# Kernel optimization log

Measured on AMD Instinct MI355X. Metric: run time of the kernel, lower is better.

Reference implementation:

```python
import jax, jax.numpy as jnp
import numpy as np

D_MODEL = 2048
N_HEAD = 16
D_HEAD = D_MODEL // N_HEAD


def setup_inputs() -> dict:
    key = jax.random.key(0)
    k_x, k_qkv, k_proj = jax.random.split(key, 3)
    x = jax.random.normal(k_x, (2, 2048, D_MODEL), dtype=jnp.float32)
    # nn.Linear weights: out = x @ W.T ; store as [out, in] like torch
    scale = 1.0 / np.sqrt(D_MODEL)
    W_qkv = jax.random.uniform(k_qkv, (3 * D_MODEL, D_MODEL), jnp.float32, -scale, scale)
    W_proj = jax.random.uniform(k_proj, (D_MODEL, D_MODEL), jnp.float32, -scale, scale)
    return {"x": x, "W_qkv": W_qkv, "W_proj": W_proj}


def reference(x, W_qkv, W_proj):
    B, T, C = x.shape
    qkv = jnp.einsum('btc,oc->bto', x, W_qkv)  # [B,T,3C]
    q, k, v = jnp.split(qkv, 3, axis=-1)
    def heads(t):
        return t.reshape(B, T, N_HEAD, D_HEAD).transpose(0, 2, 1, 3)  # [B,H,T,Dh]
    q, k, v = heads(q), heads(k), heads(v)
    att = jnp.einsum('bhqd,bhkd->bhqk', q, k) / jnp.sqrt(jnp.float32(D_HEAD))
    causal = jnp.tril(jnp.ones((T, T), dtype=bool))  # True = keep
    att = jnp.where(causal, att, -jnp.inf)
    att = jax.nn.softmax(att, axis=-1)
    y = jnp.einsum('bhqk,bhkd->bhqd', att, v)
    y = y.transpose(0, 2, 1, 3).reshape(B, T, C)
    return jnp.einsum('btc,oc->bto', y, W_proj)
```

## Files before the change

kernel.cpp:

```cpp
#include <hip/hip_runtime.h>
#include <hip/hip_bf16.h>
#include <stdint.h>


typedef __bf16 bf16x8 __attribute__((ext_vector_type(8)));
typedef float f32x4 __attribute__((ext_vector_type(4)));
typedef unsigned short u16x8 __attribute__((ext_vector_type(8)));
typedef unsigned short u16x4 __attribute__((ext_vector_type(4)));

__device__ __forceinline__ unsigned short f2bf(float f) {
  unsigned int u = __builtin_bit_cast(unsigned int, f);
  u += 0x7fff + ((u >> 16) & 1);
  return (unsigned short)(u >> 16);
}
__device__ __forceinline__ float bf2f(unsigned short u) {
  return __builtin_bit_cast(float, (unsigned int)u << 16);
}

__device__ __forceinline__ u16x8 cvt8(const float* p) {
  f32x4 lo = *(const f32x4*)p;
  f32x4 hi = *(const f32x4*)(p + 4);
  u16x8 r;
#pragma unroll
  for (int j = 0; j < 4; j++) { r[j] = f2bf(lo[j]); r[4 + j] = f2bf(hi[j]); }
  return r;
}

__device__ __forceinline__ void gload16(const void* g, void* l) {
  __builtin_amdgcn_global_load_lds(
      (const __attribute__((address_space(1))) void*)g,
      (__attribute__((address_space(3))) void*)l, 16, 0, 0);
}

__global__ __launch_bounds__(256) void f32_to_bf16(
    const float* __restrict__ src, unsigned short* __restrict__ dst, int n8) {
  int i = blockIdx.x * 256 + threadIdx.x;
  const int stride = gridDim.x * 256;
  for (; i < n8; i += stride) {
    u16x8 v = cvt8(src + (size_t)i * 8);
    *(u16x8*)&dst[(size_t)i * 8] = v;
  }
}

template <bool COF32>
__global__ __launch_bounds__(256) void gemm_bf(
    const unsigned short* __restrict__ A, const unsigned short* __restrict__ B,
    void* __restrict__ Cv, int M, int N, int K) {
  __shared__ __align__(16) unsigned short Alds[128 * 32];
  __shared__ __align__(16) unsigned short Blds[128 * 32];

  const int tid  = threadIdx.x;
  const int lane = tid & 63;
  const int w    = tid >> 6;
  const int ln   = lane & 15;
  const int kq   = lane >> 4;
  const int m0 = blockIdx.y * 128;
  const int n0 = blockIdx.x * 128;
  const int m_base = (w >> 1) * 64;
  const int n_base = (w & 1) * 64;

  f32x4 acc[4][4];
#pragma unroll
  for (int i = 0; i < 4; i++)
#pragma unroll
    for (int j = 0; j < 4; j++) acc[i][j] = {0.f, 0.f, 0.f, 0.f};

  const int c0 = tid;
  const int c1 = tid + 256;
  const unsigned short* Ag0 = A + (size_t)(m0 + (c0 >> 2)) * K + (c0 & 3) * 8;
  const unsigned short* Ag1 = A + (size_t)(m0 + (c1 >> 2)) * K + (c1 & 3) * 8;
  const unsigned short* Bg0 = B + (size_t)(n0 + (c0 >> 2)) * K + (c0 & 3) * 8;
  const unsigned short* Bg1 = B + (size_t)(n0 + (c1 >> 2)) * K + (c1 & 3) * 8;
  unsigned short* lA0 = &Alds[(size_t)w * 512];
  unsigned short* lA1 = &Alds[2048 + (size_t)w * 512];
  unsigned short* lB0 = &Blds[(size_t)w * 512];
  unsigned short* lB1 = &Blds[2048 + (size_t)w * 512];

  const int nk = K >> 5;
  for (int kt = 0; kt < nk; kt++) {
    const int ko = kt * 32;
    gload16(Ag0 + ko, lA0);
    gload16(Ag1 + ko, lA1);
    gload16(Bg0 + ko, lB0);
    gload16(Bg1 + ko, lB1);
    __syncthreads();

    bf16x8 af[4], bfr[4];
#pragma unroll
    for (int i = 0; i < 4; i++)
      af[i] = *(const bf16x8*)&Alds[(m_base + i * 16 + ln) * 32 + kq * 8];
#pragma unroll
    for (int j = 0; j < 4; j++)
      bfr[j] = *(const bf16x8*)&Blds[(n_base + j * 16 + ln) * 32 + kq * 8];
#pragma unroll
    for (int i = 0; i < 4; i++)
#pragma unroll
      for (int j = 0; j < 4; j++)
        acc[i][j] = __builtin_amdgcn_mfma_f32_16x16x32_bf16(af[i], bfr[j], acc[i][j], 0, 0, 0);
    __syncthreads();
  }

#pragma unroll
  for (int i = 0; i < 4; i++) {
    const int row_base = m0 + m_base + i * 16 + kq * 4;
#pragma unroll
    for (int j = 0; j < 4; j++) {
      const int col = n0 + n_base + j * 16 + ln;
#pragma unroll
      for (int r = 0; r < 4; r++) {
        const size_t idx = (size_t)(row_base + r) * N + col;
        if (COF32) ((float*)Cv)[idx] = acc[i][j][r];
        else       ((unsigned short*)Cv)[idx] = f2bf(acc[i][j][r]);
      }
    }
  }
}

template <bool COF32>
__global__ __launch_bounds__(512, 2) void gemm8(
    const unsigned short* __restrict__ A, const unsigned short* __restrict__ B,
    void* __restrict__ Cv, int M, int N, int K) {
  __shared__ __align__(1024) unsigned short As[2][16384];
  __shared__ __align__(1024) unsigned short Bs[2][16384];

  const int tid  = threadIdx.x;
  const int lane = tid & 63;
  const int w    = tid >> 6;
  const int ln   = lane & 15;
  const int kq   = lane >> 4;
  const int wm   = w >> 2;
  const int wn   = w & 3;
  const int m0 = blockIdx.y * 256;
  const int n0 = blockIdx.x * 256;

  const int kswz = (kq * 8) ^ ((ln & 8) << 1);

  const int lx = lane ^ (((lane >> 5) & 1) << 1);
  const int srow = w * 16 + (lx >> 2);
  const int scol = (lx & 3) * 8;
  const unsigned short* Asrc = A + (size_t)(m0 + srow) * K + scol;
  const unsigned short* Bsrc = B + (size_t)(n0 + srow) * K + scol;

  f32x4 acc[8][4];
#pragma unroll
  for (int i = 0; i < 8; i++)
#pragma unroll
    for (int j = 0; j < 4; j++) acc[i][j] = {0.f, 0.f, 0.f, 0.f};

  auto stgA = [&](int buf, int t, int h) {
    const size_t off = (size_t)t * 64 + (size_t)(h * 128) * K;
    gload16(Asrc + off,      &As[buf][h * 4096 + w * 512]);
    gload16(Asrc + off + 32, &As[buf][8192 + h * 4096 + w * 512]);
  };
  auto stgB = [&](int buf, int t, int h) {
    const size_t off = (size_t)t * 64 + (size_t)(h * 128) * K;
    gload16(Bsrc + off,      &Bs[buf][h * 4096 + w * 512]);
    gload16(Bsrc + off + 32, &Bs[buf][8192 + h * 4096 + w * 512]);
  };
  auto rdA = [&](int buf, int mi, int ks) -> bf16x8 {
    return *(const bf16x8*)&As[buf][ks * 8192 + (wm * 128 + mi * 16 + ln) * 32 + kswz];
  };
  auto rdB = [&](int buf, int nj, int ks) -> bf16x8 {
    return *(const bf16x8*)&Bs[buf][ks * 8192 + (wn * 64 + nj * 16 + ln) * 32 + kswz];
  };

  const int NT = K >> 6;

  stgA(0, 0, 0); stgA(0, 0, 1); stgB(0, 0, 0); stgB(0, 0, 1);
  stgA(1, 1, 0); stgA(1, 1, 1);
  asm volatile("s_waitcnt vmcnt(4)" ::: "memory");
  __builtin_amdgcn_s_barrier();

  bf16x8 a0[4][2], a1[4][2], b01[2][2], b23[2][2];

#pragma unroll 2
  for (int t = 0; t < NT; t++) {
    const int cur = t & 1, nxt = cur ^ 1;

#pragma unroll
    for (int i = 0; i < 4; i++) { a0[i][0] = rdA(cur, i, 0); a0[i][1] = rdA(cur, i, 1); }
#pragma unroll
    for (int j = 0; j < 2; j++) { b01[j][0] = rdB(cur, j, 0); b01[j][1] = rdB(cur, j, 1); }
    if (t + 1 < NT) stgB(nxt, t + 1, 0);
    asm volatile("s_waitcnt lgkmcnt(8)" ::: "memory");
    __builtin_amdgcn_s_barrier();
    asm volatile("s_waitcnt lgkmcnt(0)" ::: "memory");
    __builtin_amdgcn_sched_barrier(0);
    __builtin_amdgcn_s_setprio(1);
#pragma unroll
    for (int i = 0; i < 4; i++)
#pragma unroll
      for (int j = 0; j < 2; j++) {
        acc[i][j] = __builtin_amdgcn_mfma_f32_16x16x32_bf16(a0[i][0], b01[j][0], acc[i][j], 0, 0, 0);
        acc[i][j] = __builtin_amdgcn_mfma_f32_16x16x32_bf16(a0[i][1], b01[j][1], acc[i][j], 0, 0, 0);
      }
    __builtin_amdgcn_s_setprio(0);
    __builtin_amdgcn_s_barrier();

#pragma unroll
    for (int j = 0; j < 2; j++) { b23[j][0] = rdB(cur, 2 + j, 0); b23[j][1] = rdB(cur, 2 + j, 1); }
    if (t + 1 < NT) stgB(nxt, t + 1, 1);
    __builtin_amdgcn_s_barrier();
    asm volatile("s_waitcnt lgkmcnt(0)" ::: "memory");
    __builtin_amdgcn_sched_barrier(0);
    __builtin_amdgcn_s_setprio(1);
#pragma unroll
    for (int i = 0; i < 4; i++)
#pragma unroll
      for (int j = 0; j < 2; j++) {
        acc[i][2 + j] = __builtin_amdgcn_mfma_f32_16x16x32_bf16(a0[i][0], b23[j][0], acc[i][2 + j], 0, 0, 0);
        acc[i][2 + j] = __builtin_amdgcn_mfma_f32_16x16x32_bf16(a0[i][1], b23[j][1], acc[i][2 + j], 0, 0, 0);
      }
    __builtin_amdgcn_s_setprio(0);
    __builtin_amdgcn_s_barrier();

#pragma unroll
    for (int i = 0; i < 4; i++) { a1[i][0] = rdA(cur, 4 + i, 0); a1[i][1] = rdA(cur, 4 + i, 1); }
    asm volatile("s_waitcnt lgkmcnt(4)" ::: "memory");
    __builtin_amdgcn_s_barrier();
    asm volatile("s_waitcnt lgkmcnt(0)" ::: "memory");
    __builtin_amdgcn_sched_barrier(0);
    __builtin_amdgcn_s_setprio(1);
#pragma unroll
    for (int i = 0; i < 4; i++)
#pragma unroll
      for (int j = 0; j < 2; j++) {
        acc[4 + i][2 + j] = __builtin_amdgcn_mfma_f32_16x16x32_bf16(a1[i][0], b23[j][0], acc[4 + i][2 + j], 0, 0, 0);
        acc[4 + i][2 + j] = __builtin_amdgcn_mfma_f32_16x16x32_bf16(a1[i][1], b23[j][1], acc[4 + i][2 + j], 0, 0, 0);
      }
    __builtin_amdgcn_s_setprio(0);
    __builtin_amdgcn_s_barrier();

    if (t + 2 < NT) { stgA(cur, t + 2, 0); stgA(cur, t + 2, 1); }
    __builtin_amdgcn_s_barrier();
    __builtin_amdgcn_sched_barrier(0);
    __builtin_amdgcn_s_setprio(1);
#pragma unroll
    for (int i = 0; i < 4; i++)
#pragma unroll
      for (int j = 0; j < 2; j++) {
        acc[4 + i][j] = __builtin_amdgcn_mfma_f32_16x16x32_bf16(a1[i][0], b01[j][0], acc[4 + i][j], 0, 0, 0);
        acc[4 + i][j] = __builtin_amdgcn_mfma_f32_16x16x32_bf16(a1[i][1], b01[j][1], acc[4 + i][j], 0, 0, 0);
      }
    __builtin_amdgcn_s_setprio(0);
    if (t + 2 < NT) asm volatile("s_waitcnt vmcnt(4)" ::: "memory");
    else            asm volatile("s_waitcnt vmcnt(0)" ::: "memory");
    __builtin_amdgcn_s_barrier();
  }

#pragma unroll
  for (int mi = 0; mi < 8; mi++) {
    const int row_base = m0 + wm * 128 + mi * 16 + kq * 4;
#pragma unroll
    for (int nj = 0; nj < 4; nj++) {
      const int col = n0 + wn * 64 + nj * 16 + ln;
#pragma unroll
      for (int r = 0; r < 4; r++) {
        const size_t idx = (size_t)(row_base + r) * N + col;
        if (COF32) ((float*)Cv)[idx] = acc[mi][nj][r];
        else       ((unsigned short*)Cv)[idx] = f2bf(acc[mi][nj][r]);
      }
    }
  }
}

#define TSEQ 2048
#define CDIM 2048
#define QKVLD 6144
#define DH 128
#define NEG_BIG (-1.0e30f)
#define K_LD 136
#define VT_LD 76
#define P_LD 72

__global__ __launch_bounds__(512, 4) void attn(
    const unsigned short* __restrict__ qkv,
    unsigned short* __restrict__ y) {
  __shared__ __align__(16) unsigned short Klds[64 * K_LD];
  __shared__ __align__(16) unsigned short Vt[DH * VT_LD];
  __shared__ __align__(16) unsigned short Plds[8 * 16 * P_LD];

  const int tid  = threadIdx.x;
  const int lane = tid & 63;
  const int w    = tid >> 6;
  const int ln   = lane & 15;
  const int kq   = lane >> 4;

  const int idx  = blockIdx.x;
  const int half = idx >> 8;
  const int qbi  = idx & 15;
  const int qb   = half ? qbi : 15 - qbi;
  const int h    = (idx >> 4) & 15;
  const int b    = half;
  const int q0   = qb * 128;
  const int qrow = q0 + w * 16 + ln;

  const size_t baseQ = (size_t)b * TSEQ * QKVLD + (size_t)h * DH;
  const size_t baseK = baseQ + CDIM;
  const size_t baseV = baseQ + 2 * CDIM;

  bf16x8 qf[4];
  {
    const float scale = 0.08838834764831845f;
    const unsigned short* qp = qkv + baseQ + (size_t)qrow * QKVLD + kq * 8;
#pragma unroll
    for (int kc = 0; kc < 4; kc++) {
      u16x8 raw = *(const u16x8*)(qp + kc * 32);
      u16x8 t;
#pragma unroll
      for (int j = 0; j < 8; j++) t[j] = f2bf(bf2f(raw[j]) * scale);
      qf[kc] = __builtin_bit_cast(bf16x8, t);
    }
  }

  const int kRow = tid >> 4;
  const int kCol = (tid & 15) * 8;
  const int vK4  = (tid & 15) * 4;
  const int vD0  = (tid >> 4) * 4;
  const unsigned short* Kg = qkv + baseK + (size_t)kRow * QKVLD + kCol;
  const unsigned short* Vg = qkv + baseV + (size_t)vK4 * QKVLD + vD0;

  u16x8 kreg[2];
  u16x4 vreg[4];
#pragma unroll
  for (int it = 0; it < 2; it++)
    kreg[it] = *(const u16x8*)(Kg + (size_t)(it * 32) * QKVLD);
#pragma unroll
  for (int r = 0; r < 4; r++)
    vreg[r] = *(const u16x4*)(Vg + (size_t)r * QKVLD);

  f32x4 o[8];
#pragma unroll
  for (int i = 0; i < 8; i++) o[i] = {0.f, 0.f, 0.f, 0.f};
  float m = NEG_BIG, l = 0.f;
  unsigned short* pw = &Plds[w * 16 * P_LD];

  const int ktEnd   = 2 * qb + 2;
  const int myKtMax = (q0 + w * 16) >> 6;

  for (int kt = 0; kt < ktEnd; kt++) {
    __syncthreads();

#pragma unroll
    for (int it = 0; it < 2; it++)
      *(u16x8*)&Klds[(kRow + it * 32) * K_LD + kCol] = kreg[it];
#pragma unroll
    for (int j = 0; j < 4; j++) {
      u16x4 t = {vreg[0][j], vreg[1][j], vreg[2][j], vreg[3][j]};
      *(u16x4*)&Vt[(vD0 + j) * VT_LD + vK4] = t;
    }
    __syncthreads();

    if (kt + 1 < ktEnd) {
      const size_t off = (size_t)(kt + 1) * 64 * QKVLD;
#pragma unroll
      for (int it = 0; it < 2; it++)
        kreg[it] = *(const u16x8*)(Kg + off + (size_t)(it * 32) * QKVLD);
#pragma unroll
      for (int r = 0; r < 4; r++)
        vreg[r] = *(const u16x4*)(Vg + off + (size_t)r * QKVLD);
    }

    if (kt > myKtMax) continue;

    f32x4 s[4];
#pragma unroll
    for (int nt = 0; nt < 4; nt++) {
      s[nt] = {0.f, 0.f, 0.f, 0.f};
#pragma unroll
      for (int kc = 0; kc < 4; kc++) {
        bf16x8 kb = *(const bf16x8*)&Klds[(nt * 16 + ln) * K_LD + kc * 32 + kq * 8];
        s[nt] = __builtin_amdgcn_mfma_f32_16x16x32_bf16(kb, qf[kc], s[nt], 0, 0, 0);
      }
    }

    if (kt == myKtMax) {
      const int kbase = kt * 64 + kq * 4;
#pragma unroll
      for (int nt = 0; nt < 4; nt++)
#pragma unroll
        for (int r = 0; r < 4; r++)
          if (kbase + nt * 16 + r > qrow) s[nt][r] = NEG_BIG;
    }

    float mt;
    {
      f32x4 t01 = {fmaxf(s[0][0], s[0][1]), fmaxf(s[0][2], s[0][3]),
                   fmaxf(s[1][0], s[1][1]), fmaxf(s[1][2], s[1][3])};
      f32x4 t23 = {fmaxf(s[2][0], s[2][1]), fmaxf(s[2][2], s[2][3]),
                   fmaxf(s[3][0], s[3][1]), fmaxf(s[3][2], s[3][3])};
      f32x4 t = {fmaxf(t01[0], t01[1]), fmaxf(t01[2], t01[3]),
                 fmaxf(t23[0], t23[1]), fmaxf(t23[2], t23[3])};
      mt = fmaxf(fmaxf(t[0], t[1]), fmaxf(t[2], t[3]));
    }
    mt = fmaxf(mt, __shfl_xor(mt, 16, 64));
    mt = fmaxf(mt, __shfl_xor(mt, 32, 64));

    const bool defer = __all(mt - m <= 8.0f);
    const float mn = defer ? m : fmaxf(m, mt);
    const float alpha = defer ? 1.0f : __expf(m - mn);
    m = mn;

    float ps = 0.f;
#pragma unroll
    for (int nt = 0; nt < 4; nt++) {
      u16x4 pbits;
#pragma unroll
      for (int r = 0; r < 4; r++) {
        const float p = __expf(s[nt][r] - mn);
        ps += p;
        pbits[r] = f2bf(p);
      }
      *(u16x4*)&pw[ln * P_LD + nt * 16 + kq * 4] = pbits;
    }
    ps += __shfl_xor(ps, 16, 64);
    ps += __shfl_xor(ps, 32, 64);
    l = l * alpha + ps;

    if (!defer) {
#pragma unroll
      for (int i = 0; i < 8; i++)
#pragma unroll
        for (int r = 0; r < 4; r++) o[i][r] *= alpha;
    }

    bf16x8 pa[2];
#pragma unroll
    for (int kc = 0; kc < 2; kc++)
      pa[kc] = *(const bf16x8*)&pw[ln * P_LD + kc * 32 + kq * 8];
#pragma unroll
    for (int nt = 0; nt < 8; nt++)
#pragma unroll
      for (int kc = 0; kc < 2; kc++) {
        bf16x8 vb = *(const bf16x8*)&Vt[(nt * 16 + ln) * VT_LD + kc * 32 + kq * 8];
        o[nt] = __builtin_amdgcn_mfma_f32_16x16x32_bf16(vb, pa[kc], o[nt], 0, 0, 0);
      }
  }

  const float inv = 1.f / l;
  unsigned short* yp = y + (size_t)(b * TSEQ + qrow) * CDIM + (size_t)h * DH + kq * 4;
#pragma unroll
  for (int nt = 0; nt < 8; nt++) {
    u16x4 ov;
#pragma unroll
    for (int r = 0; r < 4; r++) ov[r] = f2bf(o[nt][r] * inv);
    *(u16x4*)(yp + nt * 16) = ov;
  }
}

extern "C" void kernel_launch(void* const* d_in, const int* in_sizes, int n_in,
                              void* d_out, int out_size, void* d_ws, size_t ws_size,
                              hipStream_t stream) {
  const float* x     = (const float*)d_in[0];
  const float* Wqkv  = (const float*)d_in[1];
  const float* Wproj = (const float*)d_in[2];
  void* out = d_out;

  unsigned short* qkv = (unsigned short*)d_ws;
  unsigned short* y   = qkv + (size_t)4096 * 6144;
  unsigned short* xbf = y;
  unsigned short* wbf = y + (size_t)4096 * 2048;

  f32_to_bf16<<<dim3(2048), 256, 0, stream>>>(x, xbf, (4096 * 2048) / 8);
  f32_to_bf16<<<dim3(2048), 256, 0, stream>>>(Wqkv, wbf, (6144 * 2048) / 8);
  gemm8<false><<<dim3(24, 16), 512, 0, stream>>>(xbf, wbf, qkv, 4096, 6144, 2048);
  f32_to_bf16<<<dim3(2048), 256, 0, stream>>>(Wproj, wbf, (2048 * 2048) / 8);
  attn<<<dim3(512), 512, 0, stream>>>(qkv, y);
  gemm_bf<true><<<dim3(16, 32), 256, 0, stream>>>(y, wbf, out, 4096, 2048, 2048);
}
```

Measured before the change: 385.1 us.

## Rewrite attention with 32x32 MFMA, register P, swizzled double-buffered LDS

```diff
diff --git a/kernel.cpp b/kernel.cpp
--- a/kernel.cpp
+++ b/kernel.cpp
@@ -5,8 +5,10 @@
 
 typedef __bf16 bf16x8 __attribute__((ext_vector_type(8)));
 typedef float f32x4 __attribute__((ext_vector_type(4)));
+typedef float f32x16 __attribute__((ext_vector_type(16)));
 typedef unsigned short u16x8 __attribute__((ext_vector_type(8)));
 typedef unsigned short u16x4 __attribute__((ext_vector_type(4)));
+typedef unsigned int u32x4v __attribute__((ext_vector_type(4)));
 
 __device__ __forceinline__ unsigned short f2bf(float f) {
   unsigned int u = __builtin_bit_cast(unsigned int, f);
@@ -269,22 +271,18 @@
 #define QKVLD 6144
 #define DH 128
 #define NEG_BIG (-1.0e30f)
-#define K_LD 136
-#define VT_LD 76
-#define P_LD 72
-
-__global__ __launch_bounds__(512, 4) void attn(
+
+__global__ __launch_bounds__(256, 2) void attn(
     const unsigned short* __restrict__ qkv,
     unsigned short* __restrict__ y) {
-  __shared__ __align__(16) unsigned short Klds[64 * K_LD];
-  __shared__ __align__(16) unsigned short Vt[DH * VT_LD];
-  __shared__ __align__(16) unsigned short Plds[8 * 16 * P_LD];
+  __shared__ __align__(1024) unsigned short Klds[2][8192];
+  __shared__ __align__(1024) unsigned short Vt[2][8192];
 
   const int tid  = threadIdx.x;
   const int lane = tid & 63;
   const int w    = tid >> 6;
-  const int ln   = lane & 15;
-  const int kq   = lane >> 4;
+  const int l5   = lane & 31;
+  const int hi   = lane >> 5;
 
   const int idx  = blockIdx.x;
   const int half = idx >> 8;
@@ -293,159 +291,199 @@
   const int h    = (idx >> 4) & 15;
   const int b    = half;
   const int q0   = qb * 128;
-  const int qrow = q0 + w * 16 + ln;
+  const int qcol = q0 + w * 32 + l5;
 
   const size_t baseQ = (size_t)b * TSEQ * QKVLD + (size_t)h * DH;
   const size_t baseK = baseQ + CDIM;
   const size_t baseV = baseQ + 2 * CDIM;
 
-  bf16x8 qf[4];
+  bf16x8 qf[8];
   {
     const float scale = 0.08838834764831845f;
-    const unsigned short* qp = qkv + baseQ + (size_t)qrow * QKVLD + kq * 8;
-#pragma unroll
-    for (int kc = 0; kc < 4; kc++) {
-      u16x8 raw = *(const u16x8*)(qp + kc * 32);
+    const unsigned short* qp = qkv + baseQ + (size_t)qcol * QKVLD + hi * 8;
+#pragma unroll
+    for (int c = 0; c < 8; c++) {
+      u16x8 raw = *(const u16x8*)(qp + c * 16);
       u16x8 t;
 #pragma unroll
       for (int j = 0; j < 8; j++) t[j] = f2bf(bf2f(raw[j]) * scale);
-      qf[kc] = __builtin_bit_cast(bf16x8, t);
-    }
-  }
-
-  const int kRow = tid >> 4;
-  const int kCol = (tid & 15) * 8;
-  const int vK4  = (tid & 15) * 4;
-  const int vD0  = (tid >> 4) * 4;
-  const unsigned short* Kg = qkv + baseK + (size_t)kRow * QKVLD + kCol;
-  const unsigned short* Vg = qkv + baseV + (size_t)vK4 * QKVLD + vD0;
-
-  u16x8 kreg[2];
-  u16x4 vreg[4];
-#pragma unroll
-  for (int it = 0; it < 2; it++)
-    kreg[it] = *(const u16x8*)(Kg + (size_t)(it * 32) * QKVLD);
-#pragma unroll
-  for (int r = 0; r < 4; r++)
-    vreg[r] = *(const u16x4*)(Vg + (size_t)r * QKVLD);
-
-  f32x4 o[8];
-#pragma unroll
-  for (int i = 0; i < 8; i++) o[i] = {0.f, 0.f, 0.f, 0.f};
+      qf[c] = __builtin_bit_cast(bf16x8, t);
+    }
+  }
+
+  const int kkeyb = tid >> 4;
+  const int kslot = tid & 15;
+  const int vk4 = (tid & 15) * 4;
+  const int vd8 = (tid >> 4) * 8;
+  const unsigned short* Vgb = qkv + baseV + (size_t)vk4 * QKVLD + vd8;
+
+  u16x8 vreg[4];
+
+  auto stageK = [&](int buf, int kt) {
+#pragma unroll
+    for (int it = 0; it < 4; it++) {
+      const int key = it * 16 + kkeyb;
+      const unsigned short* src = qkv + baseK + (size_t)(kt * 64 + key) * QKVLD
+                                + (size_t)((kslot ^ (key & 7)) * 8);
+      gload16(src, (char*)&Klds[buf][0] + it * 4096 + w * 1024);
+    }
+  };
+  auto loadV = [&](int kt) {
+    const size_t off = (size_t)kt * 64 * QKVLD;
+#pragma unroll
+    for (int r = 0; r < 4; r++)
+      vreg[r] = *(const u16x8*)(Vgb + off + (size_t)r * QKVLD);
+  };
+  auto writeV = [&](int buf) {
+#pragma unroll
+    for (int j = 0; j < 8; j++) {
+      const int d = vd8 + j;
+      u16x4 t4 = {vreg[0][j], vreg[1][j], vreg[2][j], vreg[3][j]};
+      *(u16x4*)((char*)&Vt[buf][0] + d * 128 + ((vk4 * 2) ^ ((d & 7) << 4))) = t4;
+    }
+  };
+  auto rdK = [&](int buf, int ks, int c) -> bf16x8 {
+    const int key = ks * 32 + l5;
+    return *(const bf16x8*)((const char*)&Klds[buf][0] + key * 256 +
+                            ((c * 32 + hi * 16) ^ ((key & 7) << 4)));
+  };
+  auto rdV = [&](int buf, int ds, int kc) -> bf16x8 {
+    const int d = ds * 32 + l5;
+    return *(const bf16x8*)((const char*)&Vt[buf][0] + d * 128 +
+                            ((kc * 32 + hi * 16) ^ ((d & 7) << 4)));
+  };
+
+  f32x16 o[4];
+#pragma unroll
+  for (int ds = 0; ds < 4; ds++)
+#pragma unroll
+    for (int r = 0; r < 16; r++) o[ds][r] = 0.f;
   float m = NEG_BIG, l = 0.f;
-  unsigned short* pw = &Plds[w * 16 * P_LD];
 
   const int ktEnd   = 2 * qb + 2;
-  const int myKtMax = (q0 + w * 16) >> 6;
+  const int myKtMax = (q0 + w * 32) >> 6;
+
+  stageK(0, 0);
+  loadV(0);
+  writeV(0);
+  __syncthreads();
 
   for (int kt = 0; kt < ktEnd; kt++) {
+    const int buf = kt & 1;
+    const bool pre = (kt + 1 < ktEnd);
+    if (pre) { stageK(buf ^ 1, kt + 1); loadV(kt + 1); }
+
+    if (kt <= myKtMax) {
+      f32x16 s0, s1;
+#pragma unroll
+      for (int r = 0; r < 16; r++) { s0[r] = 0.f; s1[r] = 0.f; }
+      __builtin_amdgcn_s_setprio(1);
+#pragma unroll
+      for (int c = 0; c < 8; c++) {
+        bf16x8 k0 = rdK(buf, 0, c);
+        bf16x8 k1 = rdK(buf, 1, c);
+        s0 = __builtin_amdgcn_mfma_f32_32x32x16_bf16(k0, qf[c], s0, 0, 0, 0);
+        s1 = __builtin_amdgcn_mfma_f32_32x32x16_bf16(k1, qf[c], s1, 0, 0, 0);
+      }
+      __builtin_amdgcn_s_setprio(0);
+
+      if (kt == myKtMax) {
+        const int kb0 = kt * 64 + 4 * hi;
+#pragma unroll
+        for (int r = 0; r < 16; r++) {
+          const int row = (r & 3) + 8 * (r >> 2) + kb0;
+          if (row > qcol)      s0[r] = NEG_BIG;
+          if (row + 32 > qcol) s1[r] = NEG_BIG;
+        }
+      }
+
+      float mt = s0[0];
+#pragma unroll
+      for (int r = 1; r < 16; r++) mt = fmaxf(mt, s0[r]);
+#pragma unroll
+      for (int r = 0; r < 16; r++) mt = fmaxf(mt, s1[r]);
+      mt = fmaxf(mt, __shfl_xor(mt, 32, 64));
+
+      const bool defer = __all(mt - m <= 8.0f);
+      const float mn = defer ? m : fmaxf(m, mt);
+      const float alpha = defer ? 1.0f : __expf(m - mn);
+      m = mn;
+
+      float ps = 0.f;
+      unsigned int w0[2][4], w1[2][4];
+#pragma unroll
+      for (int g = 0; g < 4; g++) {
+        float p0 = __expf(s0[4 * g + 0] - mn), p1 = __expf(s0[4 * g + 1] - mn);
+        float p2 = __expf(s0[4 * g + 2] - mn), p3 = __expf(s0[4 * g + 3] - mn);
+        ps += (p0 + p1) + (p2 + p3);
+        w0[0][g] = (unsigned)f2bf(p0) | ((unsigned)f2bf(p1) << 16);
+        w1[0][g] = (unsigned)f2bf(p2) | ((unsigned)f2bf(p3) << 16);
+      }
+#pragma unroll
+      for (int g = 0; g < 4; g++) {
+        float p0 = __expf(s1[4 * g + 0] - mn), p1 = __expf(s1[4 * g + 1] - mn);
+        float p2 = __expf(s1[4 * g + 2] - mn), p3 = __expf(s1[4 * g + 3] - mn);
+        ps += (p0 + p1) + (p2 + p3);
+        w0[1][g] = (unsigned)f2bf(p0) | ((unsigned)f2bf(p1) << 16);
+        w1[1][g] = (unsigned)f2bf(p2) | ((unsigned)f2bf(p3) << 16);
+      }
+      ps += __shfl_xor(ps, 32, 64);
+      l = l * alpha + ps;
+
+      if (!defer) {
+#pragma unroll
+        for (int ds = 0; ds < 4; ds++)
+#pragma unroll
+          for (int r = 0; r < 16; r++) o[ds][r] *= alpha;
+      }
+
+      unsigned int pw0[2][4], pw1[2][4];
+#pragma unroll
+      for (int ks = 0; ks < 2; ks++)
+#pragma unroll
+        for (int g = 0; g < 4; g++) {
+          pw0[ks][g] = (unsigned)__shfl_xor((int)w0[ks][g], 32, 64);
+          pw1[ks][g] = (unsigned)__shfl_xor((int)w1[ks][g], 32, 64);
+        }
+      bf16x8 pf[4];
+#pragma unroll
+      for (int kc = 0; kc < 4; kc++) {
+        const int ks = kc >> 1;
+        const int g = ((kc & 1) << 1) | hi;
+        u32x4v fw;
+        fw[0] = hi ? pw0[ks][g] : w0[ks][g];
+        fw[1] = hi ? pw1[ks][g] : w1[ks][g];
+        fw[2] = hi ? w0[ks][g] : pw0[ks][g];
+        fw[3] = hi ? w1[ks][g] : pw1[ks][g];
+        pf[kc] = __builtin_bit_cast(bf16x8, fw);
+      }
+
+      __builtin_amdgcn_s_setprio(1);
+#pragma unroll
+      for (int ds = 0; ds < 4; ds++)
+#pragma unroll
+        for (int kc = 0; kc < 4; kc++) {
+          bf16x8 vf = rdV(buf, ds, kc);
+          o[ds] = __builtin_amdgcn_mfma_f32_32x32x16_bf16(vf, pf[kc], o[ds], 0, 0, 0);
+        }
+      __builtin_amdgcn_s_setprio(0);
+    }
+
+    if (pre) writeV(buf ^ 1);
     __syncthreads();
-
-#pragma unroll
-    for (int it = 0; it < 2; it++)
-      *(u16x8*)&Klds[(kRow + it * 32) * K_LD + kCol] = kreg[it];
-#pragma unroll
-    for (int j = 0; j < 4; j++) {
-      u16x4 t = {vreg[0][j], vreg[1][j], vreg[2][j], vreg[3][j]};
-      *(u16x4*)&Vt[(vD0 + j) * VT_LD + vK4] = t;
-    }
-    __syncthreads();
-
-    if (kt + 1 < ktEnd) {
-      const size_t off = (size_t)(kt + 1) * 64 * QKVLD;
-#pragma unroll
-      for (int it = 0; it < 2; it++)
-        kreg[it] = *(const u16x8*)(Kg + off + (size_t)(it * 32) * QKVLD);
-#pragma unroll
-      for (int r = 0; r < 4; r++)
-        vreg[r] = *(const u16x4*)(Vg + off + (size_t)r * QKVLD);
-    }
-
-    if (kt > myKtMax) continue;
-
-    f32x4 s[4];
-#pragma unroll
-    for (int nt = 0; nt < 4; nt++) {
-      s[nt] = {0.f, 0.f, 0.f, 0.f};
-#pragma unroll
-      for (int kc = 0; kc < 4; kc++) {
-        bf16x8 kb = *(const bf16x8*)&Klds[(nt * 16 + ln) * K_LD + kc * 32 + kq * 8];
-        s[nt] = __builtin_amdgcn_mfma_f32_16x16x32_bf16(kb, qf[kc], s[nt], 0, 0, 0);
-      }
-    }
-
-    if (kt == myKtMax) {
-      const int kbase = kt * 64 + kq * 4;
-#pragma unroll
-      for (int nt = 0; nt < 4; nt++)
-#pragma unroll
-        for (int r = 0; r < 4; r++)
-          if (kbase + nt * 16 + r > qrow) s[nt][r] = NEG_BIG;
-    }
-
-    float mt;
-    {
-      f32x4 t01 = {fmaxf(s[0][0], s[0][1]), fmaxf(s[0][2], s[0][3]),
-                   fmaxf(s[1][0], s[1][1]), fmaxf(s[1][2], s[1][3])};
-      f32x4 t23 = {fmaxf(s[2][0], s[2][1]), fmaxf(s[2][2], s[2][3]),
-                   fmaxf(s[3][0], s[3][1]), fmaxf(s[3][2], s[3][3])};
-      f32x4 t = {fmaxf(t01[0], t01[1]), fmaxf(t01[2], t01[3]),
-                 fmaxf(t23[0], t23[1]), fmaxf(t23[2], t23[3])};
-      mt = fmaxf(fmaxf(t[0], t[1]), fmaxf(t[2], t[3]));
-    }
-    mt = fmaxf(mt, __shfl_xor(mt, 16, 64));
-    mt = fmaxf(mt, __shfl_xor(mt, 32, 64));
-
-    const bool defer = __all(mt - m <= 8.0f);
-    const float mn = defer ? m : fmaxf(m, mt);
-    const float alpha = defer ? 1.0f : __expf(m - mn);
-    m = mn;
-
-    float ps = 0.f;
-#pragma unroll
-    for (int nt = 0; nt < 4; nt++) {
-      u16x4 pbits;
-#pragma unroll
-      for (int r = 0; r < 4; r++) {
-        const float p = __expf(s[nt][r] - mn);
-        ps += p;
-        pbits[r] = f2bf(p);
-      }
-      *(u16x4*)&pw[ln * P_LD + nt * 16 + kq * 4] = pbits;
-    }
-    ps += __shfl_xor(ps, 16, 64);
-    ps += __shfl_xor(ps, 32, 64);
-    l = l * alpha + ps;
-
-    if (!defer) {
-#pragma unroll
-      for (int i = 0; i < 8; i++)
-#pragma unroll
-        for (int r = 0; r < 4; r++) o[i][r] *= alpha;
-    }
-
-    bf16x8 pa[2];
-#pragma unroll
-    for (int kc = 0; kc < 2; kc++)
-      pa[kc] = *(const bf16x8*)&pw[ln * P_LD + kc * 32 + kq * 8];
-#pragma unroll
-    for (int nt = 0; nt < 8; nt++)
-#pragma unroll
-      for (int kc = 0; kc < 2; kc++) {
-        bf16x8 vb = *(const bf16x8*)&Vt[(nt * 16 + ln) * VT_LD + kc * 32 + kq * 8];
-        o[nt] = __builtin_amdgcn_mfma_f32_16x16x32_bf16(vb, pa[kc], o[nt], 0, 0, 0);
-      }
   }
 
   const float inv = 1.f / l;
-  unsigned short* yp = y + (size_t)(b * TSEQ + qrow) * CDIM + (size_t)h * DH + kq * 4;
-#pragma unroll
-  for (int nt = 0; nt < 8; nt++) {
-    u16x4 ov;
-#pragma unroll
-    for (int r = 0; r < 4; r++) ov[r] = f2bf(o[nt][r] * inv);
-    *(u16x4*)(yp + nt * 16) = ov;
-  }
+  unsigned short* yp = y + (size_t)(b * TSEQ + qcol) * CDIM + (size_t)h * DH;
+#pragma unroll
+  for (int ds = 0; ds < 4; ds++)
+#pragma unroll
+    for (int g = 0; g < 4; g++) {
+      u16x4 ov;
+#pragma unroll
+      for (int j = 0; j < 4; j++) ov[j] = f2bf(o[ds][4 * g + j] * inv);
+      *(u16x4*)(yp + ds * 32 + 8 * g + 4 * hi) = ov;
+    }
 }
 
 extern "C" void kernel_launch(void* const* d_in, const int* in_sizes, int n_in,
@@ -465,6 +503,6 @@
   f32_to_bf16<<<dim3(2048), 256, 0, stream>>>(Wqkv, wbf, (6144 * 2048) / 8);
   gemm8<false><<<dim3(24, 16), 512, 0, stream>>>(xbf, wbf, qkv, 4096, 6144, 2048);
   f32_to_bf16<<<dim3(2048), 256, 0, stream>>>(Wproj, wbf, (2048 * 2048) / 8);
-  attn<<<dim3(512), 512, 0, stream>>>(qkv, y);
+  attn<<<dim3(512), 256, 0, stream>>>(qkv, y);
   gemm_bf<true><<<dim3(16, 32), 256, 0, stream>>>(y, wbf, out, 4096, 2048, 2048);
 }
```

Measured after the change: 438.6 us. +13.9%, slower.

## Split attention KV range across two wave halves with swizzled LDS and merge

Applied to the files above, without the earlier changes.

```diff
diff --git a/kernel.cpp b/kernel.cpp
--- a/kernel.cpp
+++ b/kernel.cpp
@@ -269,31 +269,30 @@
 #define QKVLD 6144
 #define DH 128
 #define NEG_BIG (-1.0e30f)
-#define K_LD 136
-#define VT_LD 76
-#define P_LD 72
 
 __global__ __launch_bounds__(512, 4) void attn(
     const unsigned short* __restrict__ qkv,
     unsigned short* __restrict__ y) {
-  __shared__ __align__(16) unsigned short Klds[64 * K_LD];
-  __shared__ __align__(16) unsigned short Vt[DH * VT_LD];
-  __shared__ __align__(16) unsigned short Plds[8 * 16 * P_LD];
+  __shared__ __align__(1024) char smem[81920];
+  unsigned short* Kl = (unsigned short*)smem;
+  unsigned short* Vl = (unsigned short*)(smem + 32768);
+  unsigned short* Pl = (unsigned short*)(smem + 65536);
 
   const int tid  = threadIdx.x;
   const int lane = tid & 63;
   const int w    = tid >> 6;
+  const int grp  = w & 3;
+  const int half = w >> 2;
   const int ln   = lane & 15;
   const int kq   = lane >> 4;
 
-  const int idx  = blockIdx.x;
-  const int half = idx >> 8;
-  const int qbi  = idx & 15;
-  const int qb   = half ? qbi : 15 - qbi;
-  const int h    = (idx >> 4) & 15;
-  const int b    = half;
-  const int q0   = qb * 128;
-  const int qrow = q0 + w * 16 + ln;
+  const int idx = blockIdx.x;
+  const int qti = idx & 31;
+  const int qt  = (qti & 1) ? (31 - (qti >> 1)) : (qti >> 1);
+  const int h   = (idx >> 5) & 15;
+  const int b   = idx >> 9;
+  const int q0  = qt * 64;
+  const int qrow = q0 + grp * 16 + ln;
 
   const size_t baseQ = (size_t)b * TSEQ * QKVLD + (size_t)h * DH;
   const size_t baseK = baseQ + CDIM;
@@ -313,82 +312,97 @@
     }
   }
 
-  const int kRow = tid >> 4;
-  const int kCol = (tid & 15) * 8;
-  const int vK4  = (tid & 15) * 4;
-  const int vD0  = (tid >> 4) * 4;
-  const unsigned short* Kg = qkv + baseK + (size_t)kRow * QKVLD + kCol;
+  const int c   = tid & 255;
+  const int st  = tid >> 8;
+  const int kRow = c >> 4;
+  const int kSlot = c & 15;
+  const int vK4 = (c & 15) * 4;
+  const int vD0 = (c >> 4) * 8;
+  const unsigned short* Kg = qkv + baseK + (size_t)kRow * QKVLD + kSlot * 8;
   const unsigned short* Vg = qkv + baseV + (size_t)vK4 * QKVLD + vD0;
 
-  u16x8 kreg[2];
-  u16x4 vreg[4];
-#pragma unroll
-  for (int it = 0; it < 2; it++)
-    kreg[it] = *(const u16x8*)(Kg + (size_t)(it * 32) * QKVLD);
-#pragma unroll
-  for (int r = 0; r < 4; r++)
-    vreg[r] = *(const u16x4*)(Vg + (size_t)r * QKVLD);
+  u16x8 kreg[4], vreg[4];
+  auto loadKV = [&](int kt) {
+    const size_t off = (size_t)kt * 64 * QKVLD;
+#pragma unroll
+    for (int it = 0; it < 4; it++)
+      kreg[it] = *(const u16x8*)(Kg + off + (size_t)(it * 16) * QKVLD);
+#pragma unroll
+    for (int r = 0; r < 4; r++)
+      vreg[r] = *(const u16x8*)(Vg + off + (size_t)r * QKVLD);
+  };
+  auto writeKV = [&]() {
+    char* Kb = (char*)(Kl + st * 8192);
+#pragma unroll
+    for (int it = 0; it < 4; it++) {
+      const int row = it * 16 + kRow;
+      *(u16x8*)(Kb + row * 256 + ((kSlot * 16) ^ ((row & 7) << 4))) = kreg[it];
+    }
+    char* Vb = (char*)(Vl + st * 8192);
+#pragma unroll
+    for (int j = 0; j < 8; j++) {
+      const int d = vD0 + j;
+      u16x4 t4 = {vreg[0][j], vreg[1][j], vreg[2][j], vreg[3][j]};
+      *(u16x4*)(Vb + d * 128 + ((vK4 * 2) ^ ((d & 7) << 4))) = t4;
+    }
+  };
+  auto rdK = [&](int nt, int kc) -> bf16x8 {
+    const int row = nt * 16 + ln;
+    return *(const bf16x8*)((const char*)(Kl + half * 8192) + row * 256 +
+                            ((kc * 64 + kq * 16) ^ ((row & 7) << 4)));
+  };
+  auto rdV = [&](int nt, int kc) -> bf16x8 {
+    const int d = nt * 16 + ln;
+    return *(const bf16x8*)((const char*)(Vl + half * 8192) + d * 128 +
+                            ((kc * 64 + kq * 16) ^ ((d & 7) << 4)));
+  };
+  char* pw = (char*)(Pl + w * 1024);
 
   f32x4 o[8];
 #pragma unroll
   for (int i = 0; i < 8; i++) o[i] = {0.f, 0.f, 0.f, 0.f};
   float m = NEG_BIG, l = 0.f;
-  unsigned short* pw = &Plds[w * 16 * P_LD];
-
-  const int ktEnd   = 2 * qb + 2;
-  const int myKtMax = (q0 + w * 16) >> 6;
-
-  for (int kt = 0; kt < ktEnd; kt++) {
+
+  const int nsteps = (qt >> 1) + 1;
+
+  if (st <= qt) loadKV(st);
+
+  for (int s = 0; s < nsteps; s++) {
     __syncthreads();
-
-#pragma unroll
-    for (int it = 0; it < 2; it++)
-      *(u16x8*)&Klds[(kRow + it * 32) * K_LD + kCol] = kreg[it];
-#pragma unroll
-    for (int j = 0; j < 4; j++) {
-      u16x4 t = {vreg[0][j], vreg[1][j], vreg[2][j], vreg[3][j]};
-      *(u16x4*)&Vt[(vD0 + j) * VT_LD + vK4] = t;
-    }
+    if (2 * s + st <= qt) writeKV();
     __syncthreads();
-
-    if (kt + 1 < ktEnd) {
-      const size_t off = (size_t)(kt + 1) * 64 * QKVLD;
-#pragma unroll
-      for (int it = 0; it < 2; it++)
-        kreg[it] = *(const u16x8*)(Kg + off + (size_t)(it * 32) * QKVLD);
-#pragma unroll
-      for (int r = 0; r < 4; r++)
-        vreg[r] = *(const u16x4*)(Vg + off + (size_t)r * QKVLD);
-    }
-
-    if (kt > myKtMax) continue;
-
-    f32x4 s[4];
+    const int ktn = 2 * (s + 1) + st;
+    if (ktn <= qt) loadKV(ktn);
+
+    const int kt = 2 * s + half;
+    if (kt > qt) continue;
+
+    f32x4 sS[4];
 #pragma unroll
     for (int nt = 0; nt < 4; nt++) {
-      s[nt] = {0.f, 0.f, 0.f, 0.f};
+      sS[nt] = {0.f, 0.f, 0.f, 0.f};
 #pragma unroll
       for (int kc = 0; kc < 4; kc++) {
-        bf16x8 kb = *(const bf16x8*)&Klds[(nt * 16 + ln) * K_LD + kc * 32 + kq * 8];
-        s[nt] = __builtin_amdgcn_mfma_f32_16x16x32_bf16(kb, qf[kc], s[nt], 0, 0, 0);
-      }
-    }
-
-    if (kt == myKtMax) {
+        bf16x8 kb = rdK(nt, kc);
+        sS[nt] = __builtin_amdgcn_mfma_f32_16x16x32_bf16(kb, qf[kc], sS[nt], 0, 0, 0);
+      }
+    }
+
+    if (kt == qt) {
       const int kbase = kt * 64 + kq * 4;
 #pragma unroll
       for (int nt = 0; nt < 4; nt++)
 #pragma unroll
         for (int r = 0; r < 4; r++)
-          if (kbase + nt * 16 + r > qrow) s[nt][r] = NEG_BIG;
+          if (kbase + nt * 16 + r > qrow) sS[nt][r] = NEG_BIG;
     }
 
     float mt;
     {
-      f32x4 t01 = {fmaxf(s[0][0], s[0][1]), fmaxf(s[0][2], s[0][3]),
-                   fmaxf(s[1][0], s[1][1]), fmaxf(s[1][2], s[1][3])};
-      f32x4 t23 = {fmaxf(s[2][0], s[2][1]), fmaxf(s[2][2], s[2][3]),
-                   fmaxf(s[3][0], s[3][1]), fmaxf(s[3][2], s[3][3])};
+      f32x4 t01 = {fmaxf(sS[0][0], sS[0][1]), fmaxf(sS[0][2], sS[0][3]),
+                   fmaxf(sS[1][0], sS[1][1]), fmaxf(sS[1][2], sS[1][3])};
+      f32x4 t23 = {fmaxf(sS[2][0], sS[2][1]), fmaxf(sS[2][2], sS[2][3]),
+                   fmaxf(sS[3][0], sS[3][1]), fmaxf(sS[3][2], sS[3][3])};
       f32x4 t = {fmaxf(t01[0], t01[1]), fmaxf(t01[2], t01[3]),
                  fmaxf(t23[0], t23[1]), fmaxf(t23[2], t23[3])};
       mt = fmaxf(fmaxf(t[0], t[1]), fmaxf(t[2], t[3]));
@@ -407,11 +421,11 @@
       u16x4 pbits;
 #pragma unroll
       for (int r = 0; r < 4; r++) {
-        const float p = __expf(s[nt][r] - mn);
+        const float p = __expf(sS[nt][r] - mn);
         ps += p;
         pbits[r] = f2bf(p);
       }
-      *(u16x4*)&pw[ln * P_LD + nt * 16 + kq * 4] = pbits;
+      *(u16x4*)(pw + ln * 128 + ((((nt * 2 + (kq >> 1)) ^ (ln & 7)) << 4) + ((kq & 1) * 8))) = pbits;
     }
     ps += __shfl_xor(ps, 16, 64);
     ps += __shfl_xor(ps, 32, 64);
@@ -427,24 +441,49 @@
     bf16x8 pa[2];
 #pragma unroll
     for (int kc = 0; kc < 2; kc++)
-      pa[kc] = *(const bf16x8*)&pw[ln * P_LD + kc * 32 + kq * 8];
+      pa[kc] = *(const bf16x8*)(pw + ln * 128 + (((kc * 4 + kq) ^ (ln & 7)) << 4));
 #pragma unroll
     for (int nt = 0; nt < 8; nt++)
 #pragma unroll
       for (int kc = 0; kc < 2; kc++) {
-        bf16x8 vb = *(const bf16x8*)&Vt[(nt * 16 + ln) * VT_LD + kc * 32 + kq * 8];
+        bf16x8 vb = rdV(nt, kc);
         o[nt] = __builtin_amdgcn_mfma_f32_16x16x32_bf16(vb, pa[kc], o[nt], 0, 0, 0);
       }
   }
 
-  const float inv = 1.f / l;
-  unsigned short* yp = y + (size_t)(b * TSEQ + qrow) * CDIM + (size_t)h * DH + kq * 4;
-#pragma unroll
-  for (int nt = 0; nt < 8; nt++) {
-    u16x4 ov;
-#pragma unroll
-    for (int r = 0; r < 4; r++) ov[r] = f2bf(o[nt][r] * inv);
-    *(u16x4*)(yp + nt * 16) = ov;
+  __syncthreads();
+  float* cb = (float*)smem;
+  float* ml = (float*)(smem + 65536);
+  if (half == 1) {
+    float* cg = cb + grp * 16 * 136;
+#pragma unroll
+    for (int nt = 0; nt < 8; nt++)
+      *(f32x4*)&cg[ln * 136 + nt * 16 + kq * 4] = o[nt];
+    if (kq == 0) {
+      ml[(grp * 16 + ln) * 2 + 0] = m;
+      ml[(grp * 16 + ln) * 2 + 1] = l;
+    }
+  }
+  __syncthreads();
+  if (half == 0) {
+    const float m2 = ml[(grp * 16 + ln) * 2 + 0];
+    const float l2 = ml[(grp * 16 + ln) * 2 + 1];
+    const float mx = fmaxf(m, m2);
+    const float a1 = __expf(m - mx);
+    const float a2 = __expf(m2 - mx);
+    const float L  = l * a1 + l2 * a2;
+    const float inv = 1.f / L;
+    const float* cg = cb + grp * 16 * 136;
+    unsigned short* yp = y + (size_t)(b * TSEQ + qrow) * CDIM + (size_t)h * DH + kq * 4;
+#pragma unroll
+    for (int nt = 0; nt < 8; nt++) {
+      f32x4 o2 = *(const f32x4*)&cg[ln * 136 + nt * 16 + kq * 4];
+      u16x4 ov;
+#pragma unroll
+      for (int r = 0; r < 4; r++)
+        ov[r] = f2bf((o[nt][r] * a1 + o2[r] * a2) * inv);
+      *(u16x4*)(yp + nt * 16) = ov;
+    }
   }
 }
 
@@ -465,6 +504,6 @@
   f32_to_bf16<<<dim3(2048), 256, 0, stream>>>(Wqkv, wbf, (6144 * 2048) / 8);
   gemm8<false><<<dim3(24, 16), 512, 0, stream>>>(xbf, wbf, qkv, 4096, 6144, 2048);
   f32_to_bf16<<<dim3(2048), 256, 0, stream>>>(Wproj, wbf, (2048 * 2048) / 8);
-  attn<<<dim3(512), 512, 0, stream>>>(qkv, y);
+  attn<<<dim3(1024), 512, 0, stream>>>(qkv, y);
   gemm_bf<true><<<dim3(16, 32), 256, 0, stream>>>(y, wbf, out, 4096, 2048, 2048);
 }
```

Result: slower. 454.9 us (+18.1%).
